# Optimization experiments

Hardware: AMD Instinct MI355X
Metric: run time of the kernel (lower is better)

## Reference

```python
import jax, jax.numpy as jnp
import numpy as np

INPUT_DIM = 2048
NUM_EXPERTS = 64
TOP_K = 8
BATCH = 16384


def setup_inputs() -> dict:
    key = jax.random.key(0)
    k_x, k_n, k_wg, k_bg, k_wn = jax.random.split(key, 5)
    x = jax.random.normal(k_x, (BATCH, INPUT_DIM), dtype=jnp.float32)
    noise = jax.random.normal(k_n, (BATCH, NUM_EXPERTS), dtype=jnp.float32)
    Wg = jax.random.normal(k_wg, (NUM_EXPERTS, INPUT_DIM), dtype=jnp.float32) * 0.02
    bg = jax.random.normal(k_bg, (NUM_EXPERTS,), dtype=jnp.float32) * 0.02
    Wn = jax.random.normal(k_wn, (NUM_EXPERTS, INPUT_DIM), dtype=jnp.float32) * 0.02
    return {"x": x, "noise": noise, "Wg": Wg, "bg": bg, "Wn": Wn}


def reference(x, noise, Wg, bg, Wn):
    # logits: (B, E)
    logits = jnp.einsum("bd,ed->be", x, Wg) + bg
    noise_stddev = jax.nn.softplus(jnp.einsum("bd,ed->be", x, Wn))
    noisy_logits = logits + noise * noise_stddev

    top_k_values, top_k_indices = jax.lax.top_k(noisy_logits, TOP_K)  # (B, K)
    top_k_weights = jax.nn.softmax(top_k_values, axis=-1)

    # aux losses
    dispatch = jnp.argmax(noisy_logits, axis=-1)            # (B,)
    f = jax.nn.one_hot(dispatch, NUM_EXPERTS, dtype=logits.dtype).mean(axis=0)  # (E,)
    p = jax.nn.softmax(logits, axis=-1).mean(axis=0)        # (E,)
    load_balance_loss = NUM_EXPERTS * jnp.sum(f * p)
    z_loss = jnp.mean(jax.nn.logsumexp(logits, axis=-1) ** 2)

    return top_k_weights, top_k_indices, load_balance_loss, z_loss
```

## Files before the change

kernel.cpp:

```cpp
#include <hip/hip_runtime.h>
#include <math.h>

#define IDIM 2048
#define NE   64
#define TOPK 8
#define NB   16384
#define BM   32
#define BK   64
#define NCH  (IDIM / BK)
#define NQ   4
#define KQ   512
#define NCHQ 8
#define TAU  1e-4f

#define WS_CNT 129
#define WS_LIST 130
#define WSPLIT_BYTE 66560
#define WSPLIT_REQ  (WSPLIT_BYTE + NCH * 32768)
#define PART_BYTE   (WSPLIT_BYTE + NCH * 32768)
#define SPLIT_REQ   (PART_BYTE + (size_t)NQ * NB * 128 * 4)

typedef __attribute__((ext_vector_type(8))) short bf16x8_t;
typedef __attribute__((ext_vector_type(4))) float f32x4_t;

__device__ __forceinline__ float softplusf(float v) {
    return (v > 0.f) ? (v + log1pf(expf(-v))) : log1pf(expf(v));
}
__device__ __forceinline__ double softplus_d(double v) {
    return (v > 0.0) ? (v + log1p(exp(-v))) : log1p(exp(v));
}

__device__ __forceinline__ short f2bf(float f) {
    unsigned u = __float_as_uint(f);
    unsigned r = (u + 0x7FFFu + ((u >> 16) & 1u)) >> 16;
    return (short)r;
}
__device__ __forceinline__ float bf2f(short s) {
    return __uint_as_float(((unsigned)(unsigned short)s) << 16);
}

__global__ void init_ws_kernel(float* ws) {
    int t = threadIdx.x;
    if (t < WS_LIST) ws[t] = 0.0f;
}

__device__ __forceinline__ void split8(const float4 v0, const float4 v1,
                                       bf16x8_t& H, bf16x8_t& L) {
    float fv[8] = {v0.x, v0.y, v0.z, v0.w, v1.x, v1.y, v1.z, v1.w};
    #pragma unroll
    for (int q = 0; q < 8; ++q) {
        short hb = f2bf(fv[q]);
        short lb = f2bf(fv[q] - bf2f(hb));
        H[q] = hb; L[q] = lb;
    }
}

__device__ __forceinline__ void cvt_slot(const float4 v0, const float4 v1,
                                         char* hiP, char* loP, int off) {
    bf16x8_t H, L;
    split8(v0, v1, H, L);
    *(bf16x8_t*)(hiP + off) = H;
    *(bf16x8_t*)(loP + off) = L;
}

__global__ __launch_bounds__(256) void prep_kernel(
    const float* __restrict__ Wg, const float* __restrict__ Wn,
    char* __restrict__ wsW, float* __restrict__ ws)
{
    if (blockIdx.x == 128) {
        if (threadIdx.x < WS_LIST) ws[threadIdx.x] = 0.0f;
        return;
    }
    int g = blockIdx.x * 256 + threadIdx.x;
    int t = g >> 10, i = g & 1023;
    int row = i >> 3, wslot = i & 7;
    int kslot = wslot ^ (row & 7);
    const float* src = (row < 64 ? Wg + (size_t)row * IDIM
                                 : Wn + (size_t)(row - 64) * IDIM) + t * BK + kslot * 8;
    float4 v0 = *(const float4*)src;
    float4 v1 = *(const float4*)(src + 4);
    bf16x8_t H, L;
    split8(v0, v1, H, L);
    char* dst = wsW + (size_t)t * 32768;
    *(bf16x8_t*)(dst + i * 16)         = H;
    *(bf16x8_t*)(dst + 16384 + i * 16) = L;
}

__global__ __launch_bounds__(512, 4) void gemm_quarter_kernel(
    const float* __restrict__ x, const char* __restrict__ wsW,
    float* __restrict__ part)
{
    __shared__ char smem[40960] __attribute__((aligned(16)));
    char* AH = smem;
    char* AL = smem + 4096;
    char* BH = smem + 8192;
    char* BL = smem + 24576;

    const int u   = threadIdx.x;
    const int w   = u >> 6;
    const int l   = u & 63;
    const int lr  = l & 15;
    const int lg4 = l >> 4;
    const int s7  = lr & 7;
    const int q   = blockIdx.x & 3;
    const int row0 = (blockIdx.x >> 2) * BM;
    float* pb = part + (size_t)q * NB * 128;

    const int ar  = (u >> 3) & 31;
    const int ac  = u & 7;
    const int aoff = ar * 128 + (((ac ^ (ar & 7)) & 7) << 4);
    const float* pa = x + (size_t)(row0 + ar) * IDIM + q * KQ + ac * 8;

    f32x4_t acc[2];
    #pragma unroll
    for (int mt = 0; mt < 2; ++mt) {
        f32x4_t z = {0.f, 0.f, 0.f, 0.f};
        acc[mt] = z;
    }

    float4 ra0, ra1;
    int4 w0, w1, w2, w3;

#define QLOADT(tt) { const int k0 = (tt) * BK;                                  \
    if (u < 256) { ra0 = *(const float4*)(pa + k0);                             \
                   ra1 = *(const float4*)(pa + k0 + 4); }                       \
    const char* s_ = wsW + (size_t)(q * NCHQ + (tt)) * 32768 + u * 16;          \
    w0 = *(const int4*)(s_);          w1 = *(const int4*)(s_ + 8192);           \
    w2 = *(const int4*)(s_ + 16384);  w3 = *(const int4*)(s_ + 24576); }

    QLOADT(0);

    for (int t = 0; t < NCHQ; ++t) {
        __syncthreads();
        if (u < 256) cvt_slot(ra0, ra1, AH, AL, aoff);
        *(int4*)(BH + u * 16)        = w0;
        *(int4*)(BH + 8192 + u * 16) = w1;
        *(int4*)(BL + u * 16)        = w2;
        *(int4*)(BL + 8192 + u * 16) = w3;
        if (t + 1 < NCHQ) QLOADT(t + 1);
        __syncthreads();

        #pragma unroll
        for (int ks = 0; ks < 2; ++ks) {
            const int so = (((ks * 4 + lg4) ^ s7) << 4);
            bf16x8_t ah[2], al_[2], bh, bl;
            #pragma unroll
            for (int mt = 0; mt < 2; ++mt) {
                const int o = (mt * 16 + lr) * 128 + so;
                ah[mt]  = *(const bf16x8_t*)(AH + o);
                al_[mt] = *(const bf16x8_t*)(AL + o);
            }
            {
                const int o = (w * 16 + lr) * 128 + so;
                bh = *(const bf16x8_t*)(BH + o);
                bl = *(const bf16x8_t*)(BL + o);
            }
            #pragma unroll
            for (int mt = 0; mt < 2; ++mt) {
                acc[mt] = __builtin_amdgcn_mfma_f32_16x16x32_bf16(ah[mt],  bh, acc[mt], 0, 0, 0);
                acc[mt] = __builtin_amdgcn_mfma_f32_16x16x32_bf16(ah[mt],  bl, acc[mt], 0, 0, 0);
                acc[mt] = __builtin_amdgcn_mfma_f32_16x16x32_bf16(al_[mt], bh, acc[mt], 0, 0, 0);
            }
        }
    }

    #pragma unroll
    for (int mt = 0; mt < 2; ++mt)
        #pragma unroll
        for (int r = 0; r < 4; ++r)
            pb[(size_t)(row0 + mt * 16 + lg4 * 4 + r) * 128 + (w * 16 + lr)] = acc[mt][r];
}

__global__ __launch_bounds__(512) void gating_kernel(
    const float* __restrict__ part,
    const float* __restrict__ noise, const float* __restrict__ bg,
    float* __restrict__ out_w, float* __restrict__ out_i,
    float* __restrict__ ws, int listCap)
{
    __shared__ float sP[NE];
    __shared__ float sF[NE];
    __shared__ float sZ[1];
    const int u = threadIdx.x;
    const int w = u >> 6, l = u & 63;
    const int row0 = blockIdx.x * 32;
    const float* p0 = part;
    const float* p1 = part + (size_t)NB * 128;
    const float* p2 = part + 2 * (size_t)NB * 128;
    const float* p3 = part + 3 * (size_t)NB * 128;

    if (u < NE) { sP[u] = 0.f; sF[u] = 0.f; }
    if (u == 0) sZ[0] = 0.f;
    __syncthreads();

    float pacc = 0.f, zacc = 0.f;
    #pragma unroll 1
    for (int rr = 0; rr < 4; ++rr) {
        const int grow = row0 + w * 4 + rr;
        const size_t b = (size_t)grow * 128;
        float lg   = ((p0[b + l] + p1[b + l]) + (p2[b + l] + p3[b + l])) + bg[l];
        float npre = (p0[b + 64 + l] + p1[b + 64 + l]) + (p2[b + 64 + l] + p3[b + 64 + l]);
        float vcur = fmaf(noise[(size_t)grow * NE + l], softplusf(npre), lg);

        float tkv[9]; int tki[9];
        #pragma unroll
        for (int k = 0; k < 9; ++k) {
            float mv = vcur; int mi = l;
            #pragma unroll
            for (int o = 32; o > 0; o >>= 1) {
                float ov = __shfl_xor(mv, o);
                int   oi = __shfl_xor(mi, o);
                if (ov > mv || (ov == mv && oi < mi)) { mv = ov; mi = oi; }
            }
            tkv[k] = mv; tki[k] = mi;
            if (l == mi) vcur = -1e30f;
        }

        float m0 = tkv[0], s = 0.f, wk[TOPK];
        #pragma unroll
        for (int k = 0; k < TOPK; ++k) { wk[k] = expf(tkv[k] - m0); s += wk[k]; }
        float inv = 1.f / s;
        float myw = 0.f; int myi = 0;
        #pragma unroll
        for (int k = 0; k < TOPK; ++k)
            if (l == k) { myw = wk[k] * inv; myi = tki[k]; }
        if (l < TOPK) {
            out_w[(size_t)grow * TOPK + l] = myw;
            out_i[(size_t)grow * TOPK + l] = (float)myi;
        }

        if (l == 0) {
            atomicAdd(&sF[tki[0]], 1.f);
            float ming = 1e30f;
            #pragma unroll
            for (int k = 0; k < 8; ++k) ming = fminf(ming, tkv[k] - tkv[k + 1]);
            if (ming < TAU) {
                int slot = atomicAdd((int*)&ws[WS_CNT], 1);
                if (slot < listCap) ((int*)ws)[WS_LIST + slot] = grow;
            }
        }

        float rm = lg;
        #pragma unroll
        for (int o = 32; o > 0; o >>= 1) rm = fmaxf(rm, __shfl_xor(rm, o));
        float pe = expf(lg - rm);
        float ssum = pe;
        #pragma unroll
        for (int o = 32; o > 0; o >>= 1) ssum += __shfl_xor(ssum, o);
        pacc += pe / ssum;
        if (l == 0) { float lse = rm + logf(ssum); zacc += lse * lse; }
    }

    atomicAdd(&sP[l], pacc);
    if (l == 0) atomicAdd(sZ, zacc);
    __syncthreads();
    if (u < NE) {
        atomicAdd(&ws[u],      sF[u]);
        atomicAdd(&ws[NE + u], sP[u]);
    }
    if (u == 0) atomicAdd(&ws[2 * NE], sZ[0]);
}

template<bool PRE>
__global__ __launch_bounds__(512, 4) void gate_main_kernel(
    const float* __restrict__ x, const float* __restrict__ noise,
    const float* __restrict__ Wg, const float* __restrict__ bg,
    const float* __restrict__ Wn, const char* __restrict__ wsW,
    float* __restrict__ out_w, float* __restrict__ out_i,
    float* __restrict__ ws, int listCap)
{
    __shared__ char smem[41488] __attribute__((aligned(16)));
    char* AH = smem;
    char* AL = smem + 4096;
    char* BH = smem + 8192;
    char* BL = smem + 24576;
    float* sP = (float*)(smem + 40960);
    float* sF = (float*)(smem + 41216);
    float* sZ = (float*)(smem + 41472);
    float* sL = (float*)smem;

    const int u   = threadIdx.x;
    const int w   = u >> 6;
    const int l   = u & 63;
    const int lr  = l & 15;
    const int lg4 = l >> 4;
    const int s7  = lr & 7;
    const int row0 = blockIdx.x * BM;

    if (u < NE) { sP[u] = 0.f; sF[u] = 0.f; }
    if (u == 0) sZ[0] = 0.f;

    const int ar  = (u >> 3) & 31;
    const int ac  = u & 7;
    const int aoff = ar * 128 + (((ac ^ (ar & 7)) & 7) << 4);
    const float* pa = x + (size_t)(row0 + ar) * IDIM + ac * 8;

    const int br  = u >> 3;
    const float* pg = Wg + (size_t)br * IDIM + ac * 8;
    const float* pn = Wn + (size_t)br * IDIM + ac * 8;
    const int woff = br * 128 + ((ac ^ (br & 7)) << 4);

    f32x4_t acc[2];
    #pragma unroll
    for (int mt = 0; mt < 2; ++mt) {
        f32x4_t z = {0.f, 0.f, 0.f, 0.f};
        acc[mt] = z;
    }

    float4 ra0, ra1;
    int4 w0, w1, w2, w3;
    float4 g0, g1, n0, n1;

#define LOADT(tt) { const int k0 = (tt) * BK;                                   \
    if (u < 256) { ra0 = *(const float4*)(pa + k0);                             \
                   ra1 = *(const float4*)(pa + k0 + 4); }                       \
    if constexpr (PRE) {                                                        \
        const char* s_ = wsW + (size_t)(tt) * 32768 + u * 16;                   \
        w0 = *(const int4*)(s_);          w1 = *(const int4*)(s_ + 8192);       \
        w2 = *(const int4*)(s_ + 16384);  w3 = *(const int4*)(s_ + 24576);      \
    } else {                                                                    \
        g0 = *(const float4*)(pg + k0);   g1 = *(const float4*)(pg + k0 + 4);   \
        n0 = *(const float4*)(pn + k0);   n1 = *(const float4*)(pn + k0 + 4);   \
    } }

    LOADT(0);

    for (int t = 0; t < NCH; ++t) {
        __syncthreads();
        if (u < 256) cvt_slot(ra0, ra1, AH, AL, aoff);
        if constexpr (PRE) {
            *(int4*)(BH + u * 16)        = w0;
            *(int4*)(BH + 8192 + u * 16) = w1;
            *(int4*)(BL + u * 16)        = w2;
            *(int4*)(BL + 8192 + u * 16) = w3;
        } else {
            cvt_slot(g0, g1, BH, BL, woff);
            cvt_slot(n0, n1, BH, BL, woff + 8192);
        }
        if (t + 1 < NCH) LOADT(t + 1);
        __syncthreads();

        #pragma unroll
        for (int ks = 0; ks < 2; ++ks) {
            const int so = (((ks * 4 + lg4) ^ s7) << 4);
            bf16x8_t ah[2], al_[2], bh, bl;
            #pragma unroll
            for (int mt = 0; mt < 2; ++mt) {
                const int o = (mt * 16 + lr) * 128 + so;
                ah[mt]  = *(const bf16x8_t*)(AH + o);
                al_[mt] = *(const bf16x8_t*)(AL + o);
            }
            {
                const int o = (w * 16 + lr) * 128 + so;
                bh = *(const bf16x8_t*)(BH + o);
                bl = *(const bf16x8_t*)(BL + o);
            }
            #pragma unroll
            for (int mt = 0; mt < 2; ++mt) {
                acc[mt] = __builtin_amdgcn_mfma_f32_16x16x32_bf16(ah[mt],  bh, acc[mt], 0, 0, 0);
                acc[mt] = __builtin_amdgcn_mfma_f32_16x16x32_bf16(ah[mt],  bl, acc[mt], 0, 0, 0);
                acc[mt] = __builtin_amdgcn_mfma_f32_16x16x32_bf16(al_[mt], bh, acc[mt], 0, 0, 0);
            }
        }
    }
    __syncthreads();

    #pragma unroll
    for (int mt = 0; mt < 2; ++mt)
        #pragma unroll
        for (int r = 0; r < 4; ++r)
            sL[(mt * 16 + lg4 * 4 + r) * 132 + (w * 16 + lr)] = acc[mt][r];
    __syncthreads();

    float pacc = 0.f, zacc = 0.f;
    #pragma unroll 1
    for (int rr = 0; rr < 4; ++rr) {
        const int r = w * 4 + rr;
        const int grow = row0 + r;
        float lg   = sL[r * 132 + l] + bg[l];
        float npre = sL[r * 132 + 64 + l];
        float vcur = fmaf(noise[(size_t)grow * NE + l], softplusf(npre), lg);

        float tkv[9]; int tki[9];
        #pragma unroll
        for (int k = 0; k < 9; ++k) {
            float mv = vcur; int mi = l;
            #pragma unroll
            for (int o = 32; o > 0; o >>= 1) {
                float ov = __shfl_xor(mv, o);
                int   oi = __shfl_xor(mi, o);
                if (ov > mv || (ov == mv && oi < mi)) { mv = ov; mi = oi; }
            }
            tkv[k] = mv; tki[k] = mi;
            if (l == mi) vcur = -1e30f;
        }

        float m0 = tkv[0], s = 0.f, wk[TOPK];
        #pragma unroll
        for (int k = 0; k < TOPK; ++k) { wk[k] = expf(tkv[k] - m0); s += wk[k]; }
        float inv = 1.f / s;
        float myw = 0.f; int myi = 0;
        #pragma unroll
        for (int k = 0; k < TOPK; ++k)
            if (l == k) { myw = wk[k] * inv; myi = tki[k]; }
        if (l < TOPK) {
            out_w[(size_t)grow * TOPK + l] = myw;
            out_i[(size_t)grow * TOPK + l] = (float)myi;
        }

        if (l == 0) {
            atomicAdd(&sF[tki[0]], 1.f);
            float ming = 1e30f;
            #pragma unroll
            for (int k = 0; k < 8; ++k) ming = fminf(ming, tkv[k] - tkv[k + 1]);
            if (ming < TAU) {
                int slot = atomicAdd((int*)&ws[WS_CNT], 1);
                if (slot < listCap) ((int*)ws)[WS_LIST + slot] = grow;
            }
        }

        float rm = lg;
        #pragma unroll
        for (int o = 32; o > 0; o >>= 1) rm = fmaxf(rm, __shfl_xor(rm, o));
        float pe = expf(lg - rm);
        float ssum = pe;
        #pragma unroll
        for (int o = 32; o > 0; o >>= 1) ssum += __shfl_xor(ssum, o);
        pacc += pe / ssum;
        if (l == 0) { float lse = rm + logf(ssum); zacc += lse * lse; }
    }

    atomicAdd(&sP[l], pacc);
    if (l == 0) atomicAdd(sZ, zacc);
    __syncthreads();
    if (u < NE) {
        atomicAdd(&ws[u],      sF[u]);
        atomicAdd(&ws[NE + u], sP[u]);
    }
    if (u == 0) atomicAdd(&ws[2 * NE], sZ[0]);
}

__global__ __launch_bounds__(1024) void recheck_finalize_kernel(
    const float* __restrict__ x, const float* __restrict__ noise,
    const float* __restrict__ Wg, const float* __restrict__ bg,
    const float* __restrict__ Wn,
    float* __restrict__ out_w, float* __restrict__ out_i, float* __restrict__ out_s,
    const float* __restrict__ ws, int listCap)
{
    __shared__ double sRed[128];
    const int t = threadIdx.x;

    if (blockIdx.x == 0 && t < 64) {
        float v = (ws[t] / (float)NB) * (ws[NE + t] / (float)NB);
        #pragma unroll
        for (int o = 32; o > 0; o >>= 1) v += __shfl_down(v, o);
        if (t == 0) {
            out_s[0] = (float)NE * v;
            out_s[1] = ws[2 * NE] / (float)NB;
        }
    }

    const int* wsi = (const int*)ws;
    int cnt = wsi[WS_CNT];
    if (cnt > listCap) cnt = listCap;
    if (cnt <= 0) return;

    const int wv   = t >> 6;
    const int lane = t & 63;

    for (int bi = blockIdx.x; bi < cnt; bi += gridDim.x) {
        const int row = wsi[WS_LIST + bi];
        const float* xr = x + (size_t)row * IDIM;

        float4 xv[8];
        #pragma unroll
        for (int i = 0; i < 8; ++i)
            xv[i] = *(const float4*)(xr + i * 256 + lane * 4);

        #pragma unroll 1
        for (int si = 0; si < 8; ++si) {
            const int s = wv * 8 + si;
            const float* wr = (s < 64) ? (Wg + (size_t)s * IDIM)
                                       : (Wn + (size_t)(s - 64) * IDIM);
            double a = 0.0;
            #pragma unroll
            for (int i = 0; i < 8; ++i) {
                float4 wvv = *(const float4*)(wr + i * 256 + lane * 4);
                a = fma((double)xv[i].x, (double)wvv.x, a);
                a = fma((double)xv[i].y, (double)wvv.y, a);
                a = fma((double)xv[i].z, (double)wvv.z, a);
                a = fma((double)xv[i].w, (double)wvv.w, a);
            }
            #pragma unroll
            for (int o = 32; o > 0; o >>= 1)
                a += __shfl_xor(a, o);
            if (lane == 0) sRed[s] = a;
        }
        __syncthreads();

        if (t < 64) {
            const int l64 = t;
            double g = sRed[l64];
            double n = sRed[64 + l64];
            double lgd = g + (double)bg[l64];
            double nz = (double)noise[(size_t)row * NE + l64];
            double vcur = fma(nz, softplus_d(n), lgd);

            double tkv[TOPK]; int tki[TOPK];
            #pragma unroll
            for (int k = 0; k < TOPK; ++k) {
                double mv = vcur; int mi = l64;
                #pragma unroll
                for (int o = 32; o > 0; o >>= 1) {
                    double ov = __shfl_xor(mv, o);
                    int    oi = __shfl_xor(mi, o);
                    if (ov > mv || (ov == mv && oi < mi)) { mv = ov; mi = oi; }
                }
                tkv[k] = mv; tki[k] = mi;
                if (l64 == mi) vcur = -1e300;
            }
            double m0 = tkv[0], s = 0.0, wk[TOPK];
            #pragma unroll
            for (int k = 0; k < TOPK; ++k) { wk[k] = exp(tkv[k] - m0); s += wk[k]; }
            double inv = 1.0 / s;
            float myw = 0.f; int myi = 0;
            #pragma unroll
            for (int k = 0; k < TOPK; ++k)
                if (l64 == k) { myw = (float)(wk[k] * inv); myi = tki[k]; }
            if (l64 < TOPK) {
                out_w[(size_t)row * TOPK + l64] = myw;
                out_i[(size_t)row * TOPK + l64] = (float)myi;
            }
        }
        __syncthreads();
    }
}

extern "C" void kernel_launch(void* const* d_in, const int* in_sizes, int n_in,
                              void* d_out, int out_size, void* d_ws, size_t ws_size,
                              hipStream_t stream) {
    const float* x     = (const float*)d_in[0];
    const float* noise = (const float*)d_in[1];
    const float* Wg    = (const float*)d_in[2];
    const float* bg    = (const float*)d_in[3];
    const float* Wn    = (const float*)d_in[4];
    float* out = (float*)d_out;
    float* ws  = (float*)d_ws;
    char*  wsW = (char*)d_ws + WSPLIT_BYTE;

    long cap = (long)(ws_size / 4) - WS_LIST;
    int listCap = (int)(cap < 0 ? 0 : (cap > NB ? NB : cap));
    const bool pre   = ws_size >= (size_t)WSPLIT_REQ;
    const bool split = ws_size >= (size_t)SPLIT_REQ;

    if (split) {
        float* part = (float*)((char*)d_ws + PART_BYTE);
        hipLaunchKernelGGL(prep_kernel, dim3(129), dim3(256), 0, stream, Wg, Wn, wsW, ws);
        hipLaunchKernelGGL(gemm_quarter_kernel, dim3(NQ * NB / BM), dim3(512), 0, stream,
                           x, wsW, part);
        hipLaunchKernelGGL(gating_kernel, dim3(NB / 32), dim3(512), 0, stream,
                           part, noise, bg,
                           out, out + (size_t)NB * TOPK, ws, listCap);
    } else if (pre) {
        hipLaunchKernelGGL(prep_kernel, dim3(129), dim3(256), 0, stream, Wg, Wn, wsW, ws);
        hipLaunchKernelGGL(gate_main_kernel<true>, dim3(NB / BM), dim3(512), 0, stream,
                           x, noise, Wg, bg, Wn, wsW,
                           out, out + (size_t)NB * TOPK, ws, listCap);
    } else {
        hipLaunchKernelGGL(init_ws_kernel, dim3(1), dim3(256), 0, stream, ws);
        hipLaunchKernelGGL(gate_main_kernel<false>, dim3(NB / BM), dim3(512), 0, stream,
                           x, noise, Wg, bg, Wn, wsW,
                           out, out + (size_t)NB * TOPK, ws, listCap);
    }
    hipLaunchKernelGGL(recheck_finalize_kernel, dim3(512), dim3(1024), 0, stream,
                       x, noise, Wg, bg, Wn,
                       out, out + (size_t)NB * TOPK, out + 2 * (size_t)NB * TOPK,
                       ws, listCap);
}
```

Measured before the change: 118.0 us.

## Recheck near-tie rows inline in gating kernel instead of global list

Near-tie rows in the split path are no longer appended to a global worklist for the separate recheck kernel. Each gating block now keeps its flagged rows in shared memory and recomputes them in place with an fp64 dot product, top-k and softmax. This removes the global atomic list and lets the recheck overlap with other blocks' work. The cost is extra syncthreads and fp64 work inside the gating kernel, and the recheck kernel still launches and may find an empty list.

```diff
diff --git a/kernel.cpp b/kernel.cpp
--- a/kernel.cpp
+++ b/kernel.cpp
@@ -173,13 +173,18 @@
 
 __global__ __launch_bounds__(512) void gating_kernel(
     const float* __restrict__ part,
+    const float* __restrict__ x,
+    const float* __restrict__ Wg, const float* __restrict__ Wn,
     const float* __restrict__ noise, const float* __restrict__ bg,
     float* __restrict__ out_w, float* __restrict__ out_i,
-    float* __restrict__ ws, int listCap)
+    float* __restrict__ ws)
 {
     __shared__ float sP[NE];
     __shared__ float sF[NE];
     __shared__ float sZ[1];
+    __shared__ int   sFn;
+    __shared__ int   sFlag[32];
+    __shared__ double sRedD[128];
     const int u = threadIdx.x;
     const int w = u >> 6, l = u & 63;
     const int row0 = blockIdx.x * 32;
@@ -189,7 +194,7 @@
     const float* p3 = part + 3 * (size_t)NB * 128;
 
     if (u < NE) { sP[u] = 0.f; sF[u] = 0.f; }
-    if (u == 0) sZ[0] = 0.f;
+    if (u == 0) { sZ[0] = 0.f; sFn = 0; }
     __syncthreads();
 
     float pacc = 0.f, zacc = 0.f;
@@ -234,8 +239,8 @@
             #pragma unroll
             for (int k = 0; k < 8; ++k) ming = fminf(ming, tkv[k] - tkv[k + 1]);
             if (ming < TAU) {
-                int slot = atomicAdd((int*)&ws[WS_CNT], 1);
-                if (slot < listCap) ((int*)ws)[WS_LIST + slot] = grow;
+                int slot = atomicAdd(&sFn, 1);
+                sFlag[slot] = grow;
             }
         }
 
@@ -258,6 +263,76 @@
         atomicAdd(&ws[NE + u], sP[u]);
     }
     if (u == 0) atomicAdd(&ws[2 * NE], sZ[0]);
+    __syncthreads();
+
+    const int fn = sFn;
+    #pragma unroll 1
+    for (int fi = 0; fi < fn; ++fi) {
+        const int row = sFlag[fi];
+        const float* xr = x + (size_t)row * IDIM;
+
+        float4 xv[8];
+        #pragma unroll
+        for (int i = 0; i < 8; ++i)
+            xv[i] = *(const float4*)(xr + i * 256 + l * 4);
+
+        #pragma unroll 1
+        for (int si = 0; si < 16; ++si) {
+            const int s = w * 16 + si;
+            const float* wr = (s < 64) ? (Wg + (size_t)s * IDIM)
+                                       : (Wn + (size_t)(s - 64) * IDIM);
+            double a = 0.0;
+            #pragma unroll
+            for (int i = 0; i < 8; ++i) {
+                float4 wvv = *(const float4*)(wr + i * 256 + l * 4);
+                a = fma((double)xv[i].x, (double)wvv.x, a);
+                a = fma((double)xv[i].y, (double)wvv.y, a);
+                a = fma((double)xv[i].z, (double)wvv.z, a);
+                a = fma((double)xv[i].w, (double)wvv.w, a);
+            }
+            #pragma unroll
+            for (int o = 32; o > 0; o >>= 1)
+                a += __shfl_xor(a, o);
+            if (l == 0) sRedD[s] = a;
+        }
+        __syncthreads();
+
+        if (u < 64) {
+            const int l64 = u;
+            double g = sRedD[l64];
+            double n = sRedD[64 + l64];
+            double lgd = g + (double)bg[l64];
+            double nz = (double)noise[(size_t)row * NE + l64];
+            double vcur = fma(nz, softplus_d(n), lgd);
+
+            double tkv[TOPK]; int tki[TOPK];
+            #pragma unroll
+            for (int k = 0; k < TOPK; ++k) {
+                double mv = vcur; int mi = l64;
+                #pragma unroll
+                for (int o = 32; o > 0; o >>= 1) {
+                    double ov = __shfl_xor(mv, o);
+                    int    oi = __shfl_xor(mi, o);
+                    if (ov > mv || (ov == mv && oi < mi)) { mv = ov; mi = oi; }
+                }
+                tkv[k] = mv; tki[k] = mi;
+                if (l64 == mi) vcur = -1e300;
+            }
+            double m0 = tkv[0], s = 0.0, wk[TOPK];
+            #pragma unroll
+            for (int k = 0; k < TOPK; ++k) { wk[k] = exp(tkv[k] - m0); s += wk[k]; }
+            double inv = 1.0 / s;
+            float myw = 0.f; int myi = 0;
+            #pragma unroll
+            for (int k = 0; k < TOPK; ++k)
+                if (l64 == k) { myw = (float)(wk[k] * inv); myi = tki[k]; }
+            if (l64 < TOPK) {
+                out_w[(size_t)row * TOPK + l64] = myw;
+                out_i[(size_t)row * TOPK + l64] = (float)myi;
+            }
+        }
+        __syncthreads();
+    }
 }
 
 template<bool PRE>
@@ -558,8 +633,8 @@
         hipLaunchKernelGGL(gemm_quarter_kernel, dim3(NQ * NB / BM), dim3(512), 0, stream,
                            x, wsW, part);
         hipLaunchKernelGGL(gating_kernel, dim3(NB / 32), dim3(512), 0, stream,
-                           part, noise, bg,
-                           out, out + (size_t)NB * TOPK, ws, listCap);
+                           part, x, Wg, Wn, noise, bg,
+                           out, out + (size_t)NB * TOPK, ws);
     } else if (pre) {
         hipLaunchKernelGGL(prep_kernel, dim3(129), dim3(256), 0, stream, Wg, Wn, wsW, ws);
         hipLaunchKernelGGL(gate_main_kernel<true>, dim3(NB / BM), dim3(512), 0, stream,
```

After: 183.8 us. +55.8%, slower.
